# Kernel tuning notes

Hardware: AMD Instinct MI355X
Metric: run time of the kernel (lower is better)

The kernel has to match this reference:

```python
import jax, jax.numpy as jnp
import numpy as np

D_MODEL = 1024
NUM_HEADS = 16


def setup_inputs() -> dict:
    key = jax.random.key(0)
    ks = jax.random.split(key, 5)
    std = float(np.sqrt(2.0 / (D_MODEL + D_MODEL)))
    def w(k):
        # approximate trunc_normal init with clipped normal (init only; math of fwd unaffected)
        v = jax.random.truncated_normal(k, -3.0, 3.0, (D_MODEL, D_MODEL), jnp.float32) * std
        return v
    x = jax.random.normal(ks[0], (4, 2048, D_MODEL), jnp.float32)
    return {
        "x": x,
        "wq": w(ks[1]),
        "wk": w(ks[2]),
        "wv": w(ks[3]),
        "wo": w(ks[4]),
    }


def reference(x, wq, wk, wv, wo):
    b, s, d = x.shape
    h = NUM_HEADS
    dk = d // h
    # Linear: einsum('o i, ... i -> ... o')
    def proj(w):
        y = jnp.einsum('oi,bsi->bso', w, x)
        return y.reshape(b, s, h, dk).transpose(0, 2, 1, 3)  # b h s dk
    Q, K, V = proj(wq), proj(wk), proj(wv)
    scale = 1.0 / jnp.sqrt(jnp.asarray(dk, x.dtype))
    scores = jnp.einsum('bhqd,bhkd->bhqk', Q, K) * scale
    mask = jnp.tril(jnp.ones((s, s), dtype=bool))
    scores = jnp.where(mask, scores, -jnp.inf)
    attn = jax.nn.softmax(scores, axis=-1)
    out = jnp.einsum('bhqk,bhkd->bhqd', attn, V)
    out = out.transpose(0, 2, 1, 3).reshape(b, s, d)
    return jnp.einsum('oi,bsi->bso', wo, out)
```

## Files before the change

kernel.cpp:

```cpp
#include <hip/hip_runtime.h>
#include <hip/hip_bf16.h>


typedef __bf16 bf16x8 __attribute__((ext_vector_type(8)));
typedef __bf16 bf16x4 __attribute__((ext_vector_type(4)));
typedef float  f32x4  __attribute__((ext_vector_type(4)));
typedef float  f32x16 __attribute__((ext_vector_type(16)));
typedef unsigned int u32x4_t __attribute__((ext_vector_type(4)));

#define GLOBAL_AS __attribute__((address_space(1)))
#define LDS_AS    __attribute__((address_space(3)))

__device__ __forceinline__ void gload16(const void* g, void* l) {
    __builtin_amdgcn_global_load_lds((const GLOBAL_AS void*)g, (LDS_AS void*)l, 16, 0, 0);
}

__device__ __forceinline__ unsigned int cvtpk_bf16(float lo, float hi) {
    unsigned int r;
    asm("v_cvt_pk_bf16_f32 %0, %1, %2" : "=v"(r) : "v"(lo), "v"(hi));
    return r;
}

#define WAITVM8 asm volatile("s_waitcnt vmcnt(8)" ::: "memory")
#define WAITVM0 asm volatile("s_waitcnt vmcnt(0)" ::: "memory")

__global__ __launch_bounds__(256) void cast_kernel(
    const float* __restrict__ x, const float* __restrict__ wq,
    const float* __restrict__ wk, const float* __restrict__ wv,
    const float* __restrict__ wo, __bf16* __restrict__ xb, __bf16* __restrict__ wb) {
    int bid = blockIdx.x;
    const float* src; __bf16* dst; int base;
    if (bid < 4096) {
        src = x; dst = xb; base = bid * 2048;
    } else {
        int r = bid - 4096; int wi = r >> 9;
        src = (wi == 0) ? wq : (wi == 1) ? wk : (wi == 2) ? wv : wo;
        dst = wb + wi * 1048576; base = (r & 511) * 2048;
    }
    int idx = base + threadIdx.x * 8;
    float4 a = *(const float4*)(src + idx);
    float4 b = *(const float4*)(src + idx + 4);
    bf16x8 o;
    o[0] = (__bf16)a.x; o[1] = (__bf16)a.y; o[2] = (__bf16)a.z; o[3] = (__bf16)a.w;
    o[4] = (__bf16)b.x; o[5] = (__bf16)b.y; o[6] = (__bf16)b.z; o[7] = (__bf16)b.w;
    *(bf16x8*)(dst + idx) = o;
}

__global__ __launch_bounds__(256) void gemm_qkv_kernel(
    const __bf16* __restrict__ A, const __bf16* __restrict__ W,
    __bf16* __restrict__ Qb, __bf16* __restrict__ Kb, __bf16* __restrict__ Vt,
    float qscale) {
    __shared__ __bf16 As[4096];
    __shared__ __bf16 Bs[4096];
    const int t = threadIdx.x;
    const int wid = t >> 6, lane = t & 63;
    const int g = lane >> 4, m = lane & 15;
    const int wr = wid >> 1, wc = wid & 1;
    const int cpx = gridDim.x >> 3;
    const int bid = (blockIdx.x & 7) * cpx + (blockIdx.x >> 3);
    const int mt = bid / 24, nt = bid % 24;
    const int m0 = mt * 128, n0 = nt * 128;
    const bool isV = (n0 >= 2048);

    const __bf16* gA = A + (m0 + (t >> 2)) * 1024 + (t & 3) * 8;
    const __bf16* gB = W + (n0 + (t >> 2)) * 1024 + (t & 3) * 8;
    __bf16* lA = As + wid * 512;
    __bf16* lB = Bs + wid * 512;

    const __bf16* pAf = As + (wr * 64 + m) * 32 + 8 * g;
    const __bf16* pBf = Bs + (wc * 64 + m) * 32 + 8 * g;

    f32x4 acc[4][4] = {};
    for (int kt = 0; kt < 32; ++kt) {
        __syncthreads();
        gload16(gA + kt * 32,         lA);
        gload16(gA + kt * 32 + 65536, lA + 2048);
        gload16(gB + kt * 32,         lB);
        gload16(gB + kt * 32 + 65536, lB + 2048);
        __syncthreads();
        bf16x8 af[4], bf[4];
#pragma unroll
        for (int i = 0; i < 4; ++i) af[i] = *(const bf16x8*)(pAf + i * 512);
#pragma unroll
        for (int i = 0; i < 4; ++i) bf[i] = *(const bf16x8*)(pBf + i * 512);
        if (isV) {
#pragma unroll
            for (int mi = 0; mi < 4; ++mi)
#pragma unroll
                for (int ni = 0; ni < 4; ++ni)
                    acc[mi][ni] = __builtin_amdgcn_mfma_f32_16x16x32_bf16(af[mi], bf[ni], acc[mi][ni], 0, 0, 0);
        } else {
#pragma unroll
            for (int mi = 0; mi < 4; ++mi)
#pragma unroll
                for (int ni = 0; ni < 4; ++ni)
                    acc[mi][ni] = __builtin_amdgcn_mfma_f32_16x16x32_bf16(bf[ni], af[mi], acc[mi][ni], 0, 0, 0);
        }
    }

    if (isV) {
        const int n0v = n0 - 2048;
        const int bb = m0 >> 11;
        const int sb = (m0 & 2047) + wr * 64 + 4 * g;
#pragma unroll
        for (int mi = 0; mi < 4; ++mi)
#pragma unroll
            for (int ni = 0; ni < 4; ++ni) {
                int n = n0v + wc * 64 + ni * 16 + m;
                int d = n & 63, hh = n >> 6;
                bf16x4 pk;
                pk[0] = (__bf16)(acc[mi][ni][0]); pk[1] = (__bf16)(acc[mi][ni][1]);
                pk[2] = (__bf16)(acc[mi][ni][2]); pk[3] = (__bf16)(acc[mi][ni][3]);
                *(bf16x4*)(Vt + ((bb * 16 + hh) * 64 + d) * 2048 + sb + mi * 16) = pk;
            }
    } else {
        __bf16* C = (n0 < 1024) ? Qb : Kb;
        const float sc = (n0 < 1024) ? qscale : 1.f;
        const int cb = (n0 & 1023) + wc * 64 + 4 * g;
        const int row = m0 + wr * 64 + m;
#pragma unroll
        for (int mi = 0; mi < 4; ++mi)
#pragma unroll
            for (int ni = 0; ni < 4; ++ni) {
                bf16x4 pk;
                pk[0] = (__bf16)(acc[mi][ni][0] * sc); pk[1] = (__bf16)(acc[mi][ni][1] * sc);
                pk[2] = (__bf16)(acc[mi][ni][2] * sc); pk[3] = (__bf16)(acc[mi][ni][3] * sc);
                *(bf16x4*)(C + (row + mi * 16) * 1024 + cb + ni * 16) = pk;
            }
    }
}

__global__ __launch_bounds__(256) void gemm_out_kernel(
    const __bf16* __restrict__ A, const __bf16* __restrict__ W, float* __restrict__ out) {
    __shared__ __bf16 As[4096];
    __shared__ __bf16 Bs[4096];
    const int t = threadIdx.x;
    const int wid = t >> 6, lane = t & 63;
    const int g = lane >> 4, m = lane & 15;
    const int wr = wid >> 1, wc = wid & 1;
    const int cpx = gridDim.x >> 3;
    const int bid = (blockIdx.x & 7) * cpx + (blockIdx.x >> 3);
    const int mt = bid >> 3, nt = bid & 7;
    const int m0 = mt * 128, n0 = nt * 128;

    const __bf16* gA = A + (m0 + (t >> 2)) * 1024 + (t & 3) * 8;
    const __bf16* gB = W + (n0 + (t >> 2)) * 1024 + (t & 3) * 8;
    __bf16* lA = As + wid * 512;
    __bf16* lB = Bs + wid * 512;

    const __bf16* pAf = As + (wr * 64 + m) * 32 + 8 * g;
    const __bf16* pBf = Bs + (wc * 64 + m) * 32 + 8 * g;

    f32x4 acc[4][4] = {};
    for (int kt = 0; kt < 32; ++kt) {
        __syncthreads();
        gload16(gA + kt * 32,         lA);
        gload16(gA + kt * 32 + 65536, lA + 2048);
        gload16(gB + kt * 32,         lB);
        gload16(gB + kt * 32 + 65536, lB + 2048);
        __syncthreads();
        bf16x8 af[4], bf[4];
#pragma unroll
        for (int i = 0; i < 4; ++i) af[i] = *(const bf16x8*)(pAf + i * 512);
#pragma unroll
        for (int i = 0; i < 4; ++i) bf[i] = *(const bf16x8*)(pBf + i * 512);
#pragma unroll
        for (int mi = 0; mi < 4; ++mi)
#pragma unroll
            for (int ni = 0; ni < 4; ++ni)
                acc[mi][ni] = __builtin_amdgcn_mfma_f32_16x16x32_bf16(bf[ni], af[mi], acc[mi][ni], 0, 0, 0);
    }
    const int row = m0 + wr * 64 + m;
    const int col = n0 + wc * 64 + 4 * g;
#pragma unroll
    for (int mi = 0; mi < 4; ++mi)
#pragma unroll
        for (int ni = 0; ni < 4; ++ni)
            *(f32x4*)(out + (row + mi * 16) * 1024 + col + ni * 16) = acc[mi][ni];
}

__global__ __launch_bounds__(128) void attn_kernel(
    const __bf16* __restrict__ Qb, const __bf16* __restrict__ Kb,
    const __bf16* __restrict__ Vt, __bf16* __restrict__ Ob) {
    __shared__ __align__(16) char lds[32768];
    const int t = threadIdx.x;
    const int w = t >> 6, lane = t & 63;
    const int l31 = lane & 31, hi = lane >> 5;
    const int qb = (blockIdx.x >> 3) & 15;
    const int bh = (blockIdx.x & 7) | ((blockIdx.x >> 7) << 3);
    const size_t sbase = (size_t)(bh >> 4) * 2048;
    const int hoff = (bh & 15) * 64;

    const char* Kbase = (const char*)Kb + (sbase * 1024 + hoff) * 2;
    const char* Vbase = (const char*)Vt + (size_t)bh * 262144;
    const int srow = lane >> 3;
    const int scol = ((lane & 7) ^ srow) << 4;
    const int sw = (l31 & 7) << 4;
    int colx[4];
#pragma unroll
    for (int i = 0; i < 4; ++i) colx[i] = (32 * i + 16 * hi) ^ sw;

    auto stage = [&](int kv0, char* lK) {
        char* lV = lK + 8192;
#pragma unroll
        for (int i = 0; i < 4; ++i) {
            const int chunk = i * 2 + w;
            const int row = chunk * 8 + srow;
            gload16(Kbase + (size_t)(kv0 + row) * 2048 + scol, lK + chunk * 1024);
            gload16(Vbase + (size_t)row * 4096 + (size_t)kv0 * 2 + scol, lV + chunk * 1024);
        }
    };

    for (int ph = 0; ph < 2; ++ph) {
        const int s = ph ? (31 - qb) : qb;
        const int q0w = s * 64 + w * 32;
        const int nt = s + 1;
        const int q = q0w + l31;

        const __bf16* qrow = Qb + (sbase + q0w + l31) * 1024 + hoff + 8 * hi;
        bf16x8 qf[4];
#pragma unroll
        for (int c = 0; c < 4; ++c) qf[c] = *(const bf16x8*)(qrow + 16 * c);

        f32x16 o0 = {}, o1 = {};
        float mrun = -__builtin_inff(), lrun = 0.f;

        __builtin_amdgcn_s_barrier();
        stage(0, lds);

        for (int tt = 0; tt < nt; ++tt) {
            const int cur = tt & 1;
            char* lcur = lds + cur * 16384;
            __builtin_amdgcn_s_barrier();
            if (tt + 1 < nt) {
                stage((tt + 1) * 64, lds + (cur ^ 1) * 16384);
                WAITVM8;
            } else {
                WAITVM0;
            }
            __builtin_amdgcn_s_barrier();
            __builtin_amdgcn_sched_barrier(0);

            const int kv0 = tt * 64;
            const char* lK = lcur;
            const char* lV = lcur + 8192;

            f32x16 s0 = {}, s1 = {};
            __builtin_amdgcn_s_setprio(1);
#pragma unroll
            for (int c = 0; c < 4; ++c) {
                bf16x8 k0 = *(const bf16x8*)(lK + l31 * 128 + colx[c]);
                bf16x8 k1 = *(const bf16x8*)(lK + (l31 + 32) * 128 + colx[c]);
                s0 = __builtin_amdgcn_mfma_f32_32x32x16_bf16(k0, qf[c], s0, 0, 0, 0);
                s1 = __builtin_amdgcn_mfma_f32_32x32x16_bf16(k1, qf[c], s1, 0, 0, 0);
            }
            __builtin_amdgcn_s_setprio(0);

            float p[32];
#pragma unroll
            for (int r = 0; r < 16; ++r) { p[r] = s0[r]; p[16 + r] = s1[r]; }
            if (tt == nt - 1) {
#pragma unroll
                for (int r = 0; r < 16; ++r) {
                    const int kvl = (r & 3) + 8 * (r >> 2) + 4 * hi;
                    if (kv0 + kvl > q)      p[r]      = -__builtin_inff();
                    if (kv0 + 32 + kvl > q) p[16 + r] = -__builtin_inff();
                }
            }
            float m8[8];
#pragma unroll
            for (int i = 0; i < 8; ++i)
                m8[i] = fmaxf(fmaxf(p[4 * i], p[4 * i + 1]), fmaxf(p[4 * i + 2], p[4 * i + 3]));
            float tmax = fmaxf(fmaxf(fmaxf(m8[0], m8[1]), fmaxf(m8[2], m8[3])),
                               fmaxf(fmaxf(m8[4], m8[5]), fmaxf(m8[6], m8[7])));
            const bool skip = __all(tmax <= mrun + 8.f);
            if (!skip) {
                float tq = fmaxf(tmax, __shfl_xor(tmax, 32));
                float mnew = fmaxf(mrun, tq);
                float al = __builtin_amdgcn_exp2f(mrun - mnew);
                lrun *= al;
#pragma unroll
                for (int r = 0; r < 16; ++r) { o0[r] *= al; o1[r] *= al; }
                mrun = mnew;
            }
#pragma unroll
            for (int r = 0; r < 32; ++r) p[r] = __builtin_amdgcn_exp2f(p[r] - mrun);
            float s8[8];
#pragma unroll
            for (int i = 0; i < 8; ++i)
                s8[i] = (p[4 * i] + p[4 * i + 1]) + (p[4 * i + 2] + p[4 * i + 3]);
            float rsum = ((s8[0] + s8[1]) + (s8[2] + s8[3])) + ((s8[4] + s8[5]) + (s8[6] + s8[7]));
            rsum += __shfl_xor(rsum, 32);
            lrun += rsum;

            __builtin_amdgcn_s_setprio(1);
#pragma unroll
            for (int cc = 0; cc < 4; ++cc) {
                const int pb = cc * 8;
                unsigned int A0 = cvtpk_bf16(p[pb + 0], p[pb + 1]);
                unsigned int A1 = cvtpk_bf16(p[pb + 2], p[pb + 3]);
                unsigned int B0 = cvtpk_bf16(p[pb + 4], p[pb + 5]);
                unsigned int B1 = cvtpk_bf16(p[pb + 6], p[pb + 7]);
                asm("v_permlane32_swap_b32 %0, %1" : "+v"(A0), "+v"(B0));
                asm("v_permlane32_swap_b32 %0, %1" : "+v"(A1), "+v"(B1));
                u32x4_t wvv; wvv[0] = A0; wvv[1] = A1; wvv[2] = B0; wvv[3] = B1;
                bf16x8 pa = __builtin_bit_cast(bf16x8, wvv);
                const int vcol = (32 * cc + 16 * hi) ^ sw;
                bf16x8 v0 = *(const bf16x8*)(lV + l31 * 128 + vcol);
                bf16x8 v1 = *(const bf16x8*)(lV + (l31 + 32) * 128 + vcol);
                o0 = __builtin_amdgcn_mfma_f32_32x32x16_bf16(v0, pa, o0, 0, 0, 0);
                o1 = __builtin_amdgcn_mfma_f32_32x32x16_bf16(v1, pa, o1, 0, 0, 0);
            }
            __builtin_amdgcn_s_setprio(0);
        }

        const float inv = 1.f / lrun;
        __bf16* orow = Ob + (sbase + q0w + l31) * 1024 + hoff;
#pragma unroll
        for (int rq = 0; rq < 4; ++rq) {
            bf16x4 e0, e1;
#pragma unroll
            for (int j = 0; j < 4; ++j) {
                e0[j] = (__bf16)(o0[rq * 4 + j] * inv);
                e1[j] = (__bf16)(o1[rq * 4 + j] * inv);
            }
            *(bf16x4*)(orow + 4 * hi + 8 * rq) = e0;
            *(bf16x4*)(orow + 32 + 4 * hi + 8 * rq) = e1;
        }
    }
}

extern "C" void kernel_launch(void* const* d_in, const int* in_sizes, int n_in,
                              void* d_out, int out_size, void* d_ws, size_t ws_size,
                              hipStream_t stream) {
    const float* x  = (const float*)d_in[0];
    const float* wq = (const float*)d_in[1];
    const float* wk = (const float*)d_in[2];
    const float* wv = (const float*)d_in[3];
    const float* wo = (const float*)d_in[4];

    char* ws = (char*)d_ws;
    __bf16* xb = (__bf16*)(ws);
    __bf16* wb = (__bf16*)(ws + 16777216);
    __bf16* Qb = (__bf16*)(ws + 25165824);
    __bf16* Kb = (__bf16*)(ws + 41943040);
    __bf16* Vt = (__bf16*)(ws + 58720256);
    __bf16* Ob = (__bf16*)(ws + 75497472);

    const float qscale = 0.18033688011112043f;

    cast_kernel<<<6144, 256, 0, stream>>>(x, wq, wk, wv, wo, xb, wb);
    gemm_qkv_kernel<<<1536, 256, 0, stream>>>(xb, wb, Qb, Kb, Vt, qscale);
    attn_kernel<<<1024, 128, 0, stream>>>(Qb, Kb, Vt, Ob);
    gemm_out_kernel<<<512, 256, 0, stream>>>(Ob, wb + 3145728, (float*)d_out);
}
```

Measured before the change: 193.9 us.

## Triple-buffer QKV and output GEMMs with larger 128x256 tiles and swizzled LDS

Both projection GEMMs move from 128x128 tiles with BK=32 and single-buffered LDS to 128x256 tiles with BK=64, run by 8 waves. Loads use direct global-to-LDS transfers into a three-stage ring with an XOR swizzle. Only one barrier is needed per K step, and vmcnt waits let the next stages' loads overlap the MFMA work, which also runs at raised priority. The cost is 144KB of LDS per block, which limits each CU to a single resident block and fewer blocks in the grid.

```diff
diff --git a/kernel.cpp b/kernel.cpp
--- a/kernel.cpp
+++ b/kernel.cpp
@@ -22,7 +22,9 @@
 }
 
 #define WAITVM8 asm volatile("s_waitcnt vmcnt(8)" ::: "memory")
+#define WAITVM6 asm volatile("s_waitcnt vmcnt(6)" ::: "memory")
 #define WAITVM0 asm volatile("s_waitcnt vmcnt(0)" ::: "memory")
+#define SCHEDB  __builtin_amdgcn_sched_barrier(0)
 
 __global__ __launch_bounds__(256) void cast_kernel(
     const float* __restrict__ x, const float* __restrict__ wq,
@@ -46,78 +48,125 @@
     *(bf16x8*)(dst + idx) = o;
 }
 
-__global__ __launch_bounds__(256) void gemm_qkv_kernel(
+__global__ __launch_bounds__(512, 2) void gemm_qkv_kernel(
     const __bf16* __restrict__ A, const __bf16* __restrict__ W,
     __bf16* __restrict__ Qb, __bf16* __restrict__ Kb, __bf16* __restrict__ Vt,
     float qscale) {
-    __shared__ __bf16 As[4096];
-    __shared__ __bf16 Bs[4096];
+    __shared__ __align__(16) char lds[147456];
     const int t = threadIdx.x;
     const int wid = t >> 6, lane = t & 63;
     const int g = lane >> 4, m = lane & 15;
-    const int wr = wid >> 1, wc = wid & 1;
-    const int cpx = gridDim.x >> 3;
-    const int bid = (blockIdx.x & 7) * cpx + (blockIdx.x >> 3);
-    const int mt = bid / 24, nt = bid % 24;
-    const int m0 = mt * 128, n0 = nt * 128;
+    const int wm = wid >> 2, wn = wid & 3;
+    const int bid = (blockIdx.x & 7) * 96 + (blockIdx.x >> 3);
+    const int mt = bid / 12, nt = bid % 12;
+    const int m0 = mt * 128, n0 = nt * 256;
     const bool isV = (n0 >= 2048);
 
-    const __bf16* gA = A + (m0 + (t >> 2)) * 1024 + (t & 3) * 8;
-    const __bf16* gB = W + (n0 + (t >> 2)) * 1024 + (t & 3) * 8;
-    __bf16* lA = As + wid * 512;
-    __bf16* lB = Bs + wid * 512;
-
-    const __bf16* pAf = As + (wr * 64 + m) * 32 + 8 * g;
-    const __bf16* pBf = Bs + (wc * 64 + m) * 32 + 8 * g;
+    const __bf16* sA[2]; int dA[2];
+#pragma unroll
+    for (int i = 0; i < 2; ++i) {
+        const int ci = i * 512 + t;
+        const int row = ci >> 3;
+        const int k8 = (ci & 7) ^ (row & 7);
+        sA[i] = A + (size_t)(m0 + row) * 1024 + k8 * 8;
+        dA[i] = ci * 16;
+    }
+    const __bf16* sB[4]; int dB[4];
+#pragma unroll
+    for (int i = 0; i < 4; ++i) {
+        const int ci = i * 512 + t;
+        const int row = ci >> 3;
+        const int k8 = (ci & 7) ^ (row & 7);
+        sB[i] = W + (size_t)(n0 + row) * 1024 + k8 * 8;
+        dB[i] = ci * 16;
+    }
+    auto stage = [&](int kt, char* buf) {
+        gload16(sA[0] + kt * 64, buf + dA[0]);
+        gload16(sA[1] + kt * 64, buf + dA[1]);
+        gload16(sB[0] + kt * 64, buf + 16384 + dB[0]);
+        gload16(sB[1] + kt * 64, buf + 16384 + dB[1]);
+        gload16(sB[2] + kt * 64, buf + 16384 + dB[2]);
+        gload16(sB[3] + kt * 64, buf + 16384 + dB[3]);
+    };
+
+    const int sw = (m & 7) << 4;
+    const int offA = (wm * 64 + m) * 128 + ((g << 4) ^ sw);
+    const int offB = (wn * 64 + m) * 128 + ((g << 4) ^ sw);
+
+    stage(0, lds);
+    stage(1, lds + 49152);
+    WAITVM6;
+    SCHEDB;
+    __builtin_amdgcn_s_barrier();
+    SCHEDB;
 
     f32x4 acc[4][4] = {};
-    for (int kt = 0; kt < 32; ++kt) {
-        __syncthreads();
-        gload16(gA + kt * 32,         lA);
-        gload16(gA + kt * 32 + 65536, lA + 2048);
-        gload16(gB + kt * 32,         lB);
-        gload16(gB + kt * 32 + 65536, lB + 2048);
-        __syncthreads();
-        bf16x8 af[4], bf[4];
-#pragma unroll
-        for (int i = 0; i < 4; ++i) af[i] = *(const bf16x8*)(pAf + i * 512);
-#pragma unroll
-        for (int i = 0; i < 4; ++i) bf[i] = *(const bf16x8*)(pBf + i * 512);
+    for (int kt = 0; kt < 16; ++kt) {
+        char* cbuf = lds + (kt % 3) * 49152;
+        if (kt < 14) stage(kt + 2, lds + ((kt + 2) % 3) * 49152);
+        const char* bA = cbuf;
+        const char* bB = cbuf + 16384;
+        bf16x8 a0[4], b0[4], a1[4], b1[4];
+#pragma unroll
+        for (int i = 0; i < 4; ++i) {
+            a0[i] = *(const bf16x8*)(bA + (offA + i * 2048));
+            b0[i] = *(const bf16x8*)(bB + (offB + i * 2048));
+            a1[i] = *(const bf16x8*)(bA + ((offA + i * 2048) ^ 64));
+            b1[i] = *(const bf16x8*)(bB + ((offB + i * 2048) ^ 64));
+        }
+        __builtin_amdgcn_s_setprio(1);
         if (isV) {
 #pragma unroll
             for (int mi = 0; mi < 4; ++mi)
 #pragma unroll
                 for (int ni = 0; ni < 4; ++ni)
-                    acc[mi][ni] = __builtin_amdgcn_mfma_f32_16x16x32_bf16(af[mi], bf[ni], acc[mi][ni], 0, 0, 0);
+                    acc[mi][ni] = __builtin_amdgcn_mfma_f32_16x16x32_bf16(a0[mi], b0[ni], acc[mi][ni], 0, 0, 0);
+#pragma unroll
+            for (int mi = 0; mi < 4; ++mi)
+#pragma unroll
+                for (int ni = 0; ni < 4; ++ni)
+                    acc[mi][ni] = __builtin_amdgcn_mfma_f32_16x16x32_bf16(a1[mi], b1[ni], acc[mi][ni], 0, 0, 0);
         } else {
 #pragma unroll
             for (int mi = 0; mi < 4; ++mi)
 #pragma unroll
                 for (int ni = 0; ni < 4; ++ni)
-                    acc[mi][ni] = __builtin_amdgcn_mfma_f32_16x16x32_bf16(bf[ni], af[mi], acc[mi][ni], 0, 0, 0);
+                    acc[mi][ni] = __builtin_amdgcn_mfma_f32_16x16x32_bf16(b0[ni], a0[mi], acc[mi][ni], 0, 0, 0);
+#pragma unroll
+            for (int mi = 0; mi < 4; ++mi)
+#pragma unroll
+                for (int ni = 0; ni < 4; ++ni)
+                    acc[mi][ni] = __builtin_amdgcn_mfma_f32_16x16x32_bf16(b1[ni], a1[mi], acc[mi][ni], 0, 0, 0);
+        }
+        __builtin_amdgcn_s_setprio(0);
+        if (kt < 14) { WAITVM6; }
+        else if (kt == 14) { WAITVM0; }
+        if (kt < 15) {
+            SCHEDB;
+            __builtin_amdgcn_s_barrier();
+            SCHEDB;
         }
     }
 
     if (isV) {
-        const int n0v = n0 - 2048;
         const int bb = m0 >> 11;
-        const int sb = (m0 & 2047) + wr * 64 + 4 * g;
+        const int sb = (m0 & 2047) + wm * 64 + 4 * g;
+        const int hbase = ((n0 - 2048) >> 6) + wn;
 #pragma unroll
         for (int mi = 0; mi < 4; ++mi)
 #pragma unroll
             for (int ni = 0; ni < 4; ++ni) {
-                int n = n0v + wc * 64 + ni * 16 + m;
-                int d = n & 63, hh = n >> 6;
+                const int d = ni * 16 + m;
                 bf16x4 pk;
                 pk[0] = (__bf16)(acc[mi][ni][0]); pk[1] = (__bf16)(acc[mi][ni][1]);
                 pk[2] = (__bf16)(acc[mi][ni][2]); pk[3] = (__bf16)(acc[mi][ni][3]);
-                *(bf16x4*)(Vt + ((bb * 16 + hh) * 64 + d) * 2048 + sb + mi * 16) = pk;
+                *(bf16x4*)(Vt + ((size_t)(bb * 16 + hbase) * 64 + d) * 2048 + sb + mi * 16) = pk;
             }
     } else {
         __bf16* C = (n0 < 1024) ? Qb : Kb;
         const float sc = (n0 < 1024) ? qscale : 1.f;
-        const int cb = (n0 & 1023) + wc * 64 + 4 * g;
-        const int row = m0 + wr * 64 + m;
+        const int cb = (n0 & 1023) + wn * 64 + 4 * g;
+        const int row = m0 + wm * 64 + m;
 #pragma unroll
         for (int mi = 0; mi < 4; ++mi)
 #pragma unroll
@@ -125,58 +174,102 @@
                 bf16x4 pk;
                 pk[0] = (__bf16)(acc[mi][ni][0] * sc); pk[1] = (__bf16)(acc[mi][ni][1] * sc);
                 pk[2] = (__bf16)(acc[mi][ni][2] * sc); pk[3] = (__bf16)(acc[mi][ni][3] * sc);
-                *(bf16x4*)(C + (row + mi * 16) * 1024 + cb + ni * 16) = pk;
-            }
-    }
-}
-
-__global__ __launch_bounds__(256) void gemm_out_kernel(
+                *(bf16x4*)(C + (size_t)(row + mi * 16) * 1024 + cb + ni * 16) = pk;
+            }
+    }
+}
+
+__global__ __launch_bounds__(512, 2) void gemm_out_kernel(
     const __bf16* __restrict__ A, const __bf16* __restrict__ W, float* __restrict__ out) {
-    __shared__ __bf16 As[4096];
-    __shared__ __bf16 Bs[4096];
+    __shared__ __align__(16) char lds[147456];
     const int t = threadIdx.x;
     const int wid = t >> 6, lane = t & 63;
     const int g = lane >> 4, m = lane & 15;
-    const int wr = wid >> 1, wc = wid & 1;
-    const int cpx = gridDim.x >> 3;
-    const int bid = (blockIdx.x & 7) * cpx + (blockIdx.x >> 3);
-    const int mt = bid >> 3, nt = bid & 7;
-    const int m0 = mt * 128, n0 = nt * 128;
-
-    const __bf16* gA = A + (m0 + (t >> 2)) * 1024 + (t & 3) * 8;
-    const __bf16* gB = W + (n0 + (t >> 2)) * 1024 + (t & 3) * 8;
-    __bf16* lA = As + wid * 512;
-    __bf16* lB = Bs + wid * 512;
-
-    const __bf16* pAf = As + (wr * 64 + m) * 32 + 8 * g;
-    const __bf16* pBf = Bs + (wc * 64 + m) * 32 + 8 * g;
+    const int wm = wid >> 2, wn = wid & 3;
+    const int bid = (blockIdx.x & 7) * 32 + (blockIdx.x >> 3);
+    const int mt = bid >> 2, nt = bid & 3;
+    const int m0 = mt * 128, n0 = nt * 256;
+
+    const __bf16* sA[2]; int dA[2];
+#pragma unroll
+    for (int i = 0; i < 2; ++i) {
+        const int ci = i * 512 + t;
+        const int row = ci >> 3;
+        const int k8 = (ci & 7) ^ (row & 7);
+        sA[i] = A + (size_t)(m0 + row) * 1024 + k8 * 8;
+        dA[i] = ci * 16;
+    }
+    const __bf16* sB[4]; int dB[4];
+#pragma unroll
+    for (int i = 0; i < 4; ++i) {
+        const int ci = i * 512 + t;
+        const int row = ci >> 3;
+        const int k8 = (ci & 7) ^ (row & 7);
+        sB[i] = W + (size_t)(n0 + row) * 1024 + k8 * 8;
+        dB[i] = ci * 16;
+    }
+    auto stage = [&](int kt, char* buf) {
+        gload16(sA[0] + kt * 64, buf + dA[0]);
+        gload16(sA[1] + kt * 64, buf + dA[1]);
+        gload16(sB[0] + kt * 64, buf + 16384 + dB[0]);
+        gload16(sB[1] + kt * 64, buf + 16384 + dB[1]);
+        gload16(sB[2] + kt * 64, buf + 16384 + dB[2]);
+        gload16(sB[3] + kt * 64, buf + 16384 + dB[3]);
+    };
+
+    const int sw = (m & 7) << 4;
+    const int offA = (wm * 64 + m) * 128 + ((g << 4) ^ sw);
+    const int offB = (wn * 64 + m) * 128 + ((g << 4) ^ sw);
+
+    stage(0, lds);
+    stage(1, lds + 49152);
+    WAITVM6;
+    SCHEDB;
+    __builtin_amdgcn_s_barrier();
+    SCHEDB;
 
     f32x4 acc[4][4] = {};
-    for (int kt = 0; kt < 32; ++kt) {
-        __syncthreads();
-        gload16(gA + kt * 32,         lA);
-        gload16(gA + kt * 32 + 65536, lA + 2048);
-        gload16(gB + kt * 32,         lB);
-        gload16(gB + kt * 32 + 65536, lB + 2048);
-        __syncthreads();
-        bf16x8 af[4], bf[4];
-#pragma unroll
-        for (int i = 0; i < 4; ++i) af[i] = *(const bf16x8*)(pAf + i * 512);
-#pragma unroll
-        for (int i = 0; i < 4; ++i) bf[i] = *(const bf16x8*)(pBf + i * 512);
+    for (int kt = 0; kt < 16; ++kt) {
+        char* cbuf = lds + (kt % 3) * 49152;
+        if (kt < 14) stage(kt + 2, lds + ((kt + 2) % 3) * 49152);
+        const char* bA = cbuf;
+        const char* bB = cbuf + 16384;
+        bf16x8 a0[4], b0[4], a1[4], b1[4];
+#pragma unroll
+        for (int i = 0; i < 4; ++i) {
+            a0[i] = *(const bf16x8*)(bA + (offA + i * 2048));
+            b0[i] = *(const bf16x8*)(bB + (offB + i * 2048));
+            a1[i] = *(const bf16x8*)(bA + ((offA + i * 2048) ^ 64));
+            b1[i] = *(const bf16x8*)(bB + ((offB + i * 2048) ^ 64));
+        }
+        __builtin_amdgcn_s_setprio(1);
 #pragma unroll
         for (int mi = 0; mi < 4; ++mi)
 #pragma unroll
             for (int ni = 0; ni < 4; ++ni)
-                acc[mi][ni] = __builtin_amdgcn_mfma_f32_16x16x32_bf16(bf[ni], af[mi], acc[mi][ni], 0, 0, 0);
-    }
-    const int row = m0 + wr * 64 + m;
-    const int col = n0 + wc * 64 + 4 * g;
+                acc[mi][ni] = __builtin_amdgcn_mfma_f32_16x16x32_bf16(b0[ni], a0[mi], acc[mi][ni], 0, 0, 0);
+#pragma unroll
+        for (int mi = 0; mi < 4; ++mi)
+#pragma unroll
+            for (int ni = 0; ni < 4; ++ni)
+                acc[mi][ni] = __builtin_amdgcn_mfma_f32_16x16x32_bf16(b1[ni], a1[mi], acc[mi][ni], 0, 0, 0);
+        __builtin_amdgcn_s_setprio(0);
+        if (kt < 14) { WAITVM6; }
+        else if (kt == 14) { WAITVM0; }
+        if (kt < 15) {
+            SCHEDB;
+            __builtin_amdgcn_s_barrier();
+            SCHEDB;
+        }
+    }
+
+    const int row = m0 + wm * 64 + m;
+    const int col = n0 + wn * 64 + 4 * g;
 #pragma unroll
     for (int mi = 0; mi < 4; ++mi)
 #pragma unroll
         for (int ni = 0; ni < 4; ++ni)
-            *(f32x4*)(out + (row + mi * 16) * 1024 + col + ni * 16) = acc[mi][ni];
+            *(f32x4*)(out + (size_t)(row + mi * 16) * 1024 + col + ni * 16) = acc[mi][ni];
 }
 
 __global__ __launch_bounds__(128) void attn_kernel(
@@ -350,7 +443,7 @@
     const float qscale = 0.18033688011112043f;
 
     cast_kernel<<<6144, 256, 0, stream>>>(x, wq, wk, wv, wo, xb, wb);
-    gemm_qkv_kernel<<<1536, 256, 0, stream>>>(xb, wb, Qb, Kb, Vt, qscale);
+    gemm_qkv_kernel<<<768, 512, 0, stream>>>(xb, wb, Qb, Kb, Vt, qscale);
     attn_kernel<<<1024, 128, 0, stream>>>(Qb, Kb, Vt, Ob);
-    gemm_out_kernel<<<512, 256, 0, stream>>>(Ob, wb + 3145728, (float*)d_out);
-}
+    gemm_out_kernel<<<256, 512, 0, stream>>>(Ob, wb + 3145728, (float*)d_out);
+}
```

New measurement: 188.1 us. 1.03x faster.
